# Optimization experiments

Measured on AMD Instinct MI355X. Metric: run time of the kernel, lower is better.

The kernel has to match this reference:

```python
import jax, jax.numpy as jnp
import numpy as np

DIM = 3072
HEADS = 24
HEAD_DIM = 128
MLP_HIDDEN = int(DIM * 3.0)   # 9216
EPS = 1e-6
B, S = 1, 4096


def setup_inputs() -> dict:
    key = jax.random.key(0)
    ks = jax.random.split(key, 9)
    fused_out = 3 * DIM + 2 * MLP_HIDDEN  # 27648
    std_in = 1.0 / np.sqrt(DIM)
    return {
        "hidden_states": jax.random.normal(ks[0], (B, S, DIM), jnp.float32),
        "temb_mod": jax.random.normal(ks[1], (B, 3 * DIM), jnp.float32),
        "rotary_cos": jax.random.uniform(ks[2], (S, HEAD_DIM), jnp.float32),
        "rotary_sin": jax.random.uniform(ks[3], (S, HEAD_DIM), jnp.float32),
        "w_qkv_mlp": jax.random.normal(ks[4], (DIM, fused_out), jnp.float32) * std_in,
        "w_out_attn": jax.random.normal(ks[5], (DIM, DIM), jnp.float32) * std_in,
        "w_out_mlp": jax.random.normal(ks[6], (MLP_HIDDEN, DIM), jnp.float32) * (1.0 / np.sqrt(MLP_HIDDEN)),
        "norm_q_w": jnp.ones((HEAD_DIM,), jnp.float32),
        "norm_k_w": jnp.ones((HEAD_DIM,), jnp.float32),
    }


def _rms_norm(x, w):
    var = jnp.mean(jnp.square(x), axis=-1, keepdims=True)
    return x * jax.lax.rsqrt(var + EPS) * w


def _apply_rope(x, cos, sin):
    # x: [B,H,S,D]; cos/sin: [S,D]. Interleaved (diffusers FLUX) rotation.
    xr = x.reshape(*x.shape[:-1], HEAD_DIM // 2, 2)
    x_re, x_im = xr[..., 0], xr[..., 1]
    x_rot = jnp.stack([-x_im, x_re], axis=-1).reshape(x.shape)
    return x * cos + x_rot * sin


def reference(hidden_states, temb_mod, rotary_cos, rotary_sin,
              w_qkv_mlp, w_out_attn, w_out_mlp, norm_q_w, norm_k_w):
    residual = hidden_states
    # modulation split: shift, scale, gate each [B,1,D]
    shift, scale, gate = jnp.split(temb_mod[:, None, :], 3, axis=-1)
    # LayerNorm (no affine)
    mu = jnp.mean(hidden_states, axis=-1, keepdims=True)
    var = jnp.mean(jnp.square(hidden_states - mu), axis=-1, keepdims=True)
    ln = (hidden_states - mu) * jax.lax.rsqrt(var + EPS)
    h = ln * (1.0 + scale) + shift
    # fused QKV + MLP projection
    qkv_mlp = jnp.einsum('bsd,df->bsf', h, w_qkv_mlp)
    qkv, mlp_gate_up = jnp.split(qkv_mlp, [3 * DIM], axis=-1)
    q, k, v = jnp.split(qkv, 3, axis=-1)
    to_heads = lambda t: t.reshape(B, S, HEADS, HEAD_DIM).transpose(0, 2, 1, 3)
    q, k, v = to_heads(q), to_heads(k), to_heads(v)
    q = _apply_rope(_rms_norm(q, norm_q_w), rotary_cos, rotary_sin)
    k = _apply_rope(_rms_norm(k, norm_k_w), rotary_cos, rotary_sin)
    # attention
    scores = jnp.einsum('bhqd,bhkd->bhqk', q, k) / np.sqrt(HEAD_DIM).astype(np.float32)
    attn = jnp.einsum('bhqk,bhkd->bhqd', jax.nn.softmax(scores, axis=-1), v)
    attn = attn.transpose(0, 2, 1, 3).reshape(B, S, DIM)
    # SwiGLU
    a, b = jnp.split(mlp_gate_up, 2, axis=-1)
    mlp_out = jax.nn.silu(a) * b
    out = jnp.einsum('bsd,de->bse', attn, w_out_attn) + jnp.einsum('bsm,md->bsd', mlp_out, w_out_mlp)
    return residual + gate * out
```

## Files before the change

### kernel.cpp

```cpp
#include <hip/hip_runtime.h>
#include <stdint.h>
#include <math.h>

#define DIM 3072
#define SEQ 4096
#define NH 24
#define HD 128
#define MLP 9216
#define FUSED 27648
#define SD FUSED
#define K2 12288

typedef __attribute__((ext_vector_type(8))) short short8;
typedef __attribute__((ext_vector_type(4))) float f32x4;

__device__ __forceinline__ float bf2f(uint16_t b){ uint32_t x = ((uint32_t)b)<<16; return __builtin_bit_cast(float,x); }
__device__ __forceinline__ uint16_t f2bf(float f){
  uint32_t x = __builtin_bit_cast(uint32_t,f);
  x += 0x7fffu + ((x>>16)&1u);
  return (uint16_t)(x>>16);
}
__device__ __forceinline__ void gl_lds16(const void* g, void* l){
  __builtin_amdgcn_global_load_lds((const __attribute__((address_space(1))) void*)g,
                                   (__attribute__((address_space(3))) void*)l, 16, 0, 0);
}

__global__ __launch_bounds__(256) void castT_kernel(const float* __restrict__ src,
                                                    uint16_t* __restrict__ dst,
                                                    int K, int N, int dstStride){
  __shared__ float tile[32][33];
  int t = threadIdx.x;
  int n0 = blockIdx.x<<5, k0 = blockIdx.y<<5;
  int r = t>>3, c4 = (t&7)<<2;
  float4 v = *(const float4*)&src[(size_t)(k0+r)*N + n0 + c4];
  tile[r][c4] = v.x; tile[r][c4+1] = v.y; tile[r][c4+2] = v.z; tile[r][c4+3] = v.w;
  __syncthreads();
  int n = t>>3, kc = (t&7)<<2;
  ushort4 o;
  o.x = f2bf(tile[kc  ][n]);
  o.y = f2bf(tile[kc+1][n]);
  o.z = f2bf(tile[kc+2][n]);
  o.w = f2bf(tile[kc+3][n]);
  *(ushort4*)&dst[(size_t)(n0+n)*dstStride + k0 + kc] = o;
}

__global__ __launch_bounds__(256) void ln_mod_kernel(const float* __restrict__ x,
                                                     const float* __restrict__ temb,
                                                     uint16_t* __restrict__ h){
  int s = blockIdx.x;
  int t = threadIdx.x;
  const float4* row = (const float4*)(x + (size_t)s*DIM);
  float4 v[3];
  float sum=0.f, ss=0.f;
  #pragma unroll
  for (int i=0;i<3;i++){
    v[i] = row[t + i*256];
    sum += v[i].x+v[i].y+v[i].z+v[i].w;
    ss  += v[i].x*v[i].x + v[i].y*v[i].y + v[i].z*v[i].z + v[i].w*v[i].w;
  }
  #pragma unroll
  for (int off=32; off; off>>=1){ sum += __shfl_xor(sum, off, 64); ss += __shfl_xor(ss, off, 64); }
  __shared__ float red[8];
  int lane = t&63, w = t>>6;
  if (lane==0){ red[w]=sum; red[w+4]=ss; }
  __syncthreads();
  sum = red[0]+red[1]+red[2]+red[3];
  ss  = red[4]+red[5]+red[6]+red[7];
  float mu = sum*(1.f/DIM);
  float var = ss*(1.f/DIM) - mu*mu;
  float rs = rsqrtf(var + 1e-6f);
  uint16_t* hrow = h + (size_t)s*DIM;
  #pragma unroll
  for (int i=0;i<3;i++){
    int c = (t + i*256)*4;
    float4 sc = *(const float4*)&temb[DIM + c];
    float4 sh = *(const float4*)&temb[c];
    ushort4 o;
    o.x = f2bf((v[i].x - mu)*rs*(1.f+sc.x) + sh.x);
    o.y = f2bf((v[i].y - mu)*rs*(1.f+sc.y) + sh.y);
    o.z = f2bf((v[i].z - mu)*rs*(1.f+sc.z) + sh.z);
    o.w = f2bf((v[i].w - mu)*rs*(1.f+sc.w) + sh.w);
    *(ushort4*)&hrow[c] = o;
  }
}

#define STAGE_HT(SRC, LDSB, KOFF) do{ \
    gl_lds16((SRC) + (KOFF), (LDSB) + (size_t)t*8); \
    gl_lds16((SRC) + r64K + (KOFF), (LDSB) + (size_t)(t+512)*8); \
  }while(0)

#define GPHASE(MI0, MI1, STG, WAITV) do{ \
    short8 a00 = *(const short8*)&Ab[(MI0)*1024 + pk0]; \
    short8 a01 = *(const short8*)&Ab[(MI0)*1024 + pk1]; \
    short8 a10 = *(const short8*)&Ab[(MI1)*1024 + pk0]; \
    short8 a11 = *(const short8*)&Ab[(MI1)*1024 + pk1]; \
    STG; \
    __builtin_amdgcn_s_barrier(); \
    asm volatile("s_waitcnt lgkmcnt(0)" ::: "memory"); \
    __builtin_amdgcn_s_setprio(1); \
    _Pragma("unroll") \
    for (int ni=0; ni<4; ni++){ \
      acc[MI0][ni] = __builtin_amdgcn_mfma_f32_16x16x32_bf16(a00, bfr[ni][0], acc[MI0][ni], 0,0,0); \
      acc[MI1][ni] = __builtin_amdgcn_mfma_f32_16x16x32_bf16(a10, bfr[ni][0], acc[MI1][ni], 0,0,0); \
      acc[MI0][ni] = __builtin_amdgcn_mfma_f32_16x16x32_bf16(a01, bfr[ni][1], acc[MI0][ni], 0,0,0); \
      acc[MI1][ni] = __builtin_amdgcn_mfma_f32_16x16x32_bf16(a11, bfr[ni][1], acc[MI1][ni], 0,0,0); \
    } \
    __builtin_amdgcn_s_setprio(0); \
    WAITV \
    __builtin_amdgcn_s_barrier(); \
  }while(0)

template<bool OUT_BF16, bool FINAL>
__global__ __launch_bounds__(512,2) void gemm256_kernel(const uint16_t* __restrict__ A,
                                                        const uint16_t* __restrict__ BT,
                                                        void* __restrict__ Cout,
                                                        const float* __restrict__ resid,
                                                        const float* __restrict__ temb,
                                                        int M, int N, int K){
  __shared__ alignas(16) uint16_t As[2][2][128*64];
  __shared__ alignas(16) uint16_t Bs[2][2][128*64];
  const int t = threadIdx.x, lane = t&63, w = t>>6;
  const int G = gridDim.x, cpx = G>>3;
  const int b = blockIdx.x;
  const int b2 = (b&7)*cpx + (b>>3);
  const int mt = M>>8;
  const int n_t = b2/mt, m_t = b2 - n_t*mt;
  const size_t m0 = (size_t)m_t<<8, n0 = (size_t)n_t<<8;
  const int wm = (w>>2)<<7, wn = (w&3)<<6;
  const int lr = lane&15, q4 = lane>>4;
  const int r0 = t>>3;
  const int g0 = (t&7) ^ (r0&7);
  const uint16_t* Asrc = A  + (m0 + r0)*(size_t)K + g0*8;
  const uint16_t* Bsrc = BT + (n0 + r0)*(size_t)K + g0*8;
  const size_t r64K = (size_t)64*K, r128K = (size_t)128*K;
  const int halfA = w>>2, halfB = (w&3)>>1, rbB = wn&64;
  const uint16_t* ArdBase = &As[0][halfA][0] + lr*64;
  const uint16_t* BrdBase = &Bs[0][halfB][0] + (rbB+lr)*64;
  const int x7 = lr&7;
  const int pk0 = (q4^x7)<<3, pk1 = ((q4|4)^x7)<<3;
  STAGE_HT(Bsrc, &Bs[0][0][0], (size_t)0);
  STAGE_HT(Bsrc, &Bs[0][1][0], r128K);
  STAGE_HT(Asrc, &As[0][0][0], (size_t)0);
  STAGE_HT(Asrc, &As[0][1][0], r128K);
  STAGE_HT(Bsrc, &Bs[1][0][0], (size_t)64);
  STAGE_HT(Bsrc, &Bs[1][1][0], r128K + 64);
  asm volatile("s_waitcnt vmcnt(4)" ::: "memory");
  __builtin_amdgcn_s_barrier();
  f32x4 acc[8][4] = {};
  const int NT = K>>6;
  for (int T=0; T<NT; ++T){
    const int cur = T&1, nxt = cur^1;
    const uint16_t* Ab = ArdBase + (cur<<14);
    const uint16_t* Bb = BrdBase + (cur<<14);
    uint16_t* AsN0 = &As[nxt][0][0]; uint16_t* AsN1 = &As[nxt][1][0];
    uint16_t* BsC0 = &Bs[cur][0][0]; uint16_t* BsC1 = &Bs[cur][1][0];
    const bool stA = (T+1<NT), stB = (T+2<NT);
    const size_t kA = (size_t)(T+1)<<6, kB = (size_t)(T+2)<<6;
    short8 bfr[4][2];
    #pragma unroll
    for (int ni=0; ni<4; ni++){
      bfr[ni][0] = *(const short8*)&Bb[ni*1024 + pk0];
      bfr[ni][1] = *(const short8*)&Bb[ni*1024 + pk1];
    }
    GPHASE(0,1, if(stA){ STAGE_HT(Asrc, AsN0, kA); }, ;);
    GPHASE(2,3, if(stA){ STAGE_HT(Asrc, AsN1, kA + r128K); }, ;);
    GPHASE(4,5, if(stB){ STAGE_HT(Bsrc, BsC0, kB); }, ;);
    GPHASE(6,7, if(stB){ STAGE_HT(Bsrc, BsC1, kB + r128K); },
           if(stB){ asm volatile("s_waitcnt vmcnt(4)" ::: "memory"); }
           else   { asm volatile("s_waitcnt vmcnt(0)" ::: "memory"); });
  }
  #pragma unroll
  for (int mi=0; mi<8; mi++){
    #pragma unroll
    for (int ni=0; ni<4; ni++){
      const size_t col = n0 + wn + ni*16 + lr;
      const float gate = FINAL ? temb[2*DIM + col] : 0.f;
      #pragma unroll
      for (int r=0; r<4; r++){
        const size_t row = m0 + wm + mi*16 + (q4<<2) + r;
        const size_t idx = row*(size_t)N + col;
        float vv = acc[mi][ni][r];
        if (FINAL) vv = resid[idx] + gate*vv;
        if (OUT_BF16) ((uint16_t*)Cout)[idx] = f2bf(vv);
        else          ((float*)Cout)[idx] = vv;
      }
    }
  }
}

__global__ __launch_bounds__(256) void qk_rope_kernel(uint16_t* __restrict__ qkv,
                                                      const float* __restrict__ cosb,
                                                      const float* __restrict__ sinb,
                                                      const float* __restrict__ wq,
                                                      const float* __restrict__ wk){
  int t = threadIdx.x, lane = t&63, w = t>>6;
  int pair = blockIdx.x*4 + w;
  int s = pair/24, hh = pair - s*24;
  int d0 = lane*2;
  float c0 = cosb[s*HD + d0], c1 = cosb[s*HD + d0+1];
  float sn0 = sinb[s*HD + d0], sn1 = sinb[s*HD + d0+1];
  #pragma unroll
  for (int which=0; which<2; ++which){
    uint16_t* p = qkv + (size_t)s*SD + which*DIM + hh*HD + d0;
    const float* ww = which ? wk : wq;
    uint32_t u = *(const uint32_t*)p;
    float x0 = bf2f((uint16_t)(u&0xffffu)), x1 = bf2f((uint16_t)(u>>16));
    float ssum = x0*x0 + x1*x1;
    #pragma unroll
    for (int off=32; off; off>>=1) ssum += __shfl_xor(ssum, off, 64);
    float r = rsqrtf(ssum*(1.f/HD) + 1e-6f);
    float xn0 = x0*r*ww[d0], xn1 = x1*r*ww[d0+1];
    float y0 = xn0*c0 - xn1*sn0;
    float y1 = xn1*c1 + xn0*sn1;
    *(uint32_t*)p = (uint32_t)f2bf(y0) | ((uint32_t)f2bf(y1)<<16);
  }
}

__global__ __launch_bounds__(256) void attn_kernel(const uint16_t* __restrict__ qkv,
                                                   uint16_t* __restrict__ out){
  __shared__ alignas(16) uint16_t QP[64*128];
  __shared__ alignas(16) uint16_t Ks[64*128];
  __shared__ alignas(16) uint16_t Vt[128*64];
  int t = threadIdx.x, lane = t&63, w = t>>6;
  int q0 = blockIdx.x<<6, h = blockIdx.y;
  int lr = lane&15, q4 = lane>>4, lk = q4<<3;
  const uint16_t* qb = qkv + (size_t)q0*SD + h*HD;
  #pragma unroll
  for (int i=0;i<4;i++){
    int c = t + i*256;
    gl_lds16((const char*)(qb + (size_t)(c>>4)*SD) + ((c&15)<<4), (char*)QP + c*16);
  }
  __syncthreads();
  short8 qf[4];
  #pragma unroll
  for (int kc=0;kc<4;kc++) qf[kc] = *(const short8*)&QP[(w*16+lr)*128 + kc*32 + lk];
  __syncthreads();
  float m_i[4] = {-3.0e38f,-3.0e38f,-3.0e38f,-3.0e38f};
  float l_i[4] = {0.f,0.f,0.f,0.f};
  f32x4 o[8] = {};
  const uint16_t* kb = qkv + (size_t)DIM + h*HD;
  const uint16_t* vb = qkv + (size_t)(2*DIM) + h*HD;
  uint16_t* Pw = QP + w*(16*64);
  const float scale = 0.08838834764831845f;
  for (int kt=0; kt<64; ++kt){
    const uint16_t* kbt = kb + (size_t)(kt<<6)*SD;
    const uint16_t* vbt = vb + (size_t)(kt<<6)*SD;
    __syncthreads();
    #pragma unroll
    for (int i=0;i<4;i++){
      int c = t + i*256;
      int row = c>>4, gd = c&15;
      uint4 vv = *(const uint4*)(kbt + (size_t)row*SD + gd*8);
      *(uint4*)&Ks[row*128 + ((gd ^ (row&15))<<3)] = vv;
    }
    #pragma unroll
    for (int i=0;i<8;i++){
      int idx = t + i*256;
      int rp = idx>>6;
      int k0 = rp<<1, d0 = lane<<1;
      uint32_t u0 = *(const uint32_t*)(vbt + (size_t)k0*SD + d0);
      uint32_t u1 = *(const uint32_t*)(vbt + (size_t)(k0+1)*SD + d0);
      int pos = (((rp>>2) ^ (lane&7))<<3) + (k0&7);
      *(uint32_t*)&Vt[(d0<<6) + pos]     = (u0&0xffffu) | (u1<<16);
      *(uint32_t*)&Vt[((d0+1)<<6) + pos] = (u0>>16) | (u1&0xffff0000u);
    }
    __syncthreads();
    f32x4 sa[4];
    #pragma unroll
    for (int nk=0;nk<4;nk++){
      sa[nk] = (f32x4){0.f,0.f,0.f,0.f};
      #pragma unroll
      for (int kc=0;kc<4;kc++){
        short8 kf = *(const short8*)&Ks[(nk*16+lr)*128 + (((kc*4+q4) ^ lr)<<3)];
        sa[nk] = __builtin_amdgcn_mfma_f32_16x16x32_bf16(qf[kc], kf, sa[nk], 0,0,0);
      }
      sa[nk] *= scale;
    }
    float alpha[4], psum[4];
    #pragma unroll
    for (int r=0;r<4;r++){
      float mx = fmaxf(fmaxf(sa[0][r], sa[1][r]), fmaxf(sa[2][r], sa[3][r]));
      mx = fmaxf(mx, __shfl_xor(mx, 1, 64));
      mx = fmaxf(mx, __shfl_xor(mx, 2, 64));
      mx = fmaxf(mx, __shfl_xor(mx, 4, 64));
      mx = fmaxf(mx, __shfl_xor(mx, 8, 64));
      float mn = fmaxf(m_i[r], mx);
      alpha[r] = __expf(m_i[r] - mn);
      m_i[r] = mn;
      psum[r] = 0.f;
    }
    int prow = q4<<2;
    #pragma unroll
    for (int nk=0;nk<4;nk++){
      #pragma unroll
      for (int r=0;r<4;r++){
        float p = __expf(sa[nk][r] - m_i[r]);
        psum[r] += p;
        int key = nk*16 + lr;
        Pw[(prow+r)*64 + ((((key>>3) ^ (prow+r))&7)<<3) + (key&7)] = f2bf(p);
      }
    }
    #pragma unroll
    for (int r=0;r<4;r++){
      float ps = psum[r];
      ps += __shfl_xor(ps, 1, 64);
      ps += __shfl_xor(ps, 2, 64);
      ps += __shfl_xor(ps, 4, 64);
      ps += __shfl_xor(ps, 8, 64);
      l_i[r] = l_i[r]*alpha[r] + ps;
    }
    #pragma unroll
    for (int nd=0;nd<8;nd++){
      f32x4 t4 = o[nd];
      t4[0]*=alpha[0]; t4[1]*=alpha[1]; t4[2]*=alpha[2]; t4[3]*=alpha[3];
      o[nd]=t4;
    }
    #pragma unroll
    for (int kc=0;kc<2;kc++){
      short8 pf = *(const short8*)&Pw[lr*64 + ((((kc*4+q4) ^ lr)&7)<<3)];
      #pragma unroll
      for (int nd=0;nd<8;nd++){
        int d = nd*16 + lr;
        short8 vf = *(const short8*)&Vt[(d<<6) + ((((kc*4+q4) ^ ((lr>>1)&7)))<<3)];
        o[nd] = __builtin_amdgcn_mfma_f32_16x16x32_bf16(pf, vf, o[nd], 0,0,0);
      }
    }
  }
  uint16_t* ob = out + (size_t)(q0 + w*16)*K2 + h*HD;
  #pragma unroll
  for (int r=0;r<4;r++){
    float inv = 1.f/l_i[r];
    #pragma unroll
    for (int nd=0;nd<8;nd++)
      ob[(size_t)(q4*4 + r)*K2 + nd*16 + lr] = f2bf(o[nd][r]*inv);
  }
}

__global__ __launch_bounds__(256) void swiglu_kernel(const uint16_t* __restrict__ qkv,
                                                     uint16_t* __restrict__ mlp){
  size_t idx = ((size_t)blockIdx.x*256 + threadIdx.x)*4;
  size_t s = idx/MLP, j = idx - s*MLP;
  const uint16_t* pa = qkv + s*SD + 3*DIM + j;
  const uint16_t* pb = pa + MLP;
  ushort4 ua = *(const ushort4*)pa, ub = *(const ushort4*)pb;
  ushort4 o;
  float a, b;
  a = bf2f(ua.x); b = bf2f(ub.x); o.x = f2bf(a*b/(1.f+__expf(-a)));
  a = bf2f(ua.y); b = bf2f(ub.y); o.y = f2bf(a*b/(1.f+__expf(-a)));
  a = bf2f(ua.z); b = bf2f(ub.z); o.z = f2bf(a*b/(1.f+__expf(-a)));
  a = bf2f(ua.w); b = bf2f(ub.w); o.w = f2bf(a*b/(1.f+__expf(-a)));
  *(ushort4*)(mlp + s*K2 + j) = o;
}

extern "C" void kernel_launch(void* const* d_in, const int* in_sizes, int n_in,
                              void* d_out, int out_size, void* d_ws, size_t ws_size,
                              hipStream_t stream){
  (void)in_sizes; (void)n_in; (void)out_size;
  const float* hs   = (const float*)d_in[0];
  const float* temb = (const float*)d_in[1];
  const float* rcos = (const float*)d_in[2];
  const float* rsin = (const float*)d_in[3];
  const float* w1   = (const float*)d_in[4];
  const float* wa   = (const float*)d_in[5];
  const float* wm   = (const float*)d_in[6];
  const float* nqw  = (const float*)d_in[7];
  const float* nkw  = (const float*)d_in[8];

  char* ws = (char*)d_ws;
  const size_t off_w1T  = 0;
  const size_t off_woT  = 169869312ULL;
  const size_t off_h    = 245366784ULL;
  const size_t off_qkv  = 270532608ULL;
  const size_t off_ap   = 497025024ULL;
  const size_t needed   = 597688320ULL;
  if (ws_size < needed) return;

  uint16_t* w1T  = (uint16_t*)(ws + off_w1T);
  uint16_t* woT  = (uint16_t*)(ws + off_woT);
  uint16_t* hbuf = (uint16_t*)(ws + off_h);
  uint16_t* qkv  = (uint16_t*)(ws + off_qkv);
  uint16_t* ap   = (uint16_t*)(ws + off_ap);

  castT_kernel<<<dim3(FUSED/32, DIM/32), 256, 0, stream>>>(w1, w1T, DIM, FUSED, DIM);
  castT_kernel<<<dim3(DIM/32,  DIM/32),  256, 0, stream>>>(wa, woT, DIM, DIM, K2);
  castT_kernel<<<dim3(DIM/32,  MLP/32),  256, 0, stream>>>(wm, woT + DIM, MLP, DIM, K2);
  ln_mod_kernel<<<SEQ, 256, 0, stream>>>(hs, temb, hbuf);
  gemm256_kernel<true,false><<<(SEQ/256)*(FUSED/256), 512, 0, stream>>>(hbuf, w1T, qkv, nullptr, nullptr, SEQ, FUSED, DIM);
  qk_rope_kernel<<<SEQ*NH/4, 256, 0, stream>>>(qkv, rcos, rsin, nqw, nkw);
  attn_kernel<<<dim3(SEQ/64, NH), 256, 0, stream>>>(qkv, ap);
  swiglu_kernel<<<(SEQ*(size_t)MLP/4)/256, 256, 0, stream>>>(qkv, ap + DIM);
  gemm256_kernel<false,true><<<(SEQ/256)*(DIM/256), 512, 0, stream>>>(ap, woT, d_out, hs, temb, SEQ, DIM, K2);
}
```

Baseline: 2.415 ms.

## Software-pipeline LDS fragment reads across GEMM MFMA phases with register double-buffering

Restructures the GEMM main loop so each phase's A fragments are read from LDS into a second register set while the previous phase's MFMAs run. The next tile's A and B fragments are prefetched at the end of each iteration. sched_barrier is added to keep the compiler from reordering around the phase boundaries. The aim is to hide LDS read latency behind matrix math, at the cost of more VGPRs. The prefetch of the next tile now happens before the workgroup barrier, which risks reading LDS that other waves have not finished filling.

```diff
diff --git a/kernel.cpp b/kernel.cpp
--- a/kernel.cpp
+++ b/kernel.cpp
@@ -89,26 +89,30 @@
     gl_lds16((SRC) + r64K + (KOFF), (LDSB) + (size_t)(t+512)*8); \
   }while(0)
 
-#define GPHASE(MI0, MI1, STG, WAITV) do{ \
-    short8 a00 = *(const short8*)&Ab[(MI0)*1024 + pk0]; \
-    short8 a01 = *(const short8*)&Ab[(MI0)*1024 + pk1]; \
-    short8 a10 = *(const short8*)&Ab[(MI1)*1024 + pk0]; \
-    short8 a11 = *(const short8*)&Ab[(MI1)*1024 + pk1]; \
-    STG; \
-    __builtin_amdgcn_s_barrier(); \
-    asm volatile("s_waitcnt lgkmcnt(0)" ::: "memory"); \
-    __builtin_amdgcn_s_setprio(1); \
+#define PH_READ4(d0,d1,d2,d3, BASE, MIA, MIB) \
+    d0 = *(const short8*)&(BASE)[(MIA)*1024 + pk0]; \
+    d1 = *(const short8*)&(BASE)[(MIA)*1024 + pk1]; \
+    d2 = *(const short8*)&(BASE)[(MIB)*1024 + pk0]; \
+    d3 = *(const short8*)&(BASE)[(MIB)*1024 + pk1];
+
+#define PH_MFMA4(s0,s1,s2,s3, MI0, MI1) \
     _Pragma("unroll") \
     for (int ni=0; ni<4; ni++){ \
-      acc[MI0][ni] = __builtin_amdgcn_mfma_f32_16x16x32_bf16(a00, bfr[ni][0], acc[MI0][ni], 0,0,0); \
-      acc[MI1][ni] = __builtin_amdgcn_mfma_f32_16x16x32_bf16(a10, bfr[ni][0], acc[MI1][ni], 0,0,0); \
-      acc[MI0][ni] = __builtin_amdgcn_mfma_f32_16x16x32_bf16(a01, bfr[ni][1], acc[MI0][ni], 0,0,0); \
-      acc[MI1][ni] = __builtin_amdgcn_mfma_f32_16x16x32_bf16(a11, bfr[ni][1], acc[MI1][ni], 0,0,0); \
-    } \
+      acc[MI0][ni] = __builtin_amdgcn_mfma_f32_16x16x32_bf16(s0, bfr[ni][0], acc[MI0][ni], 0,0,0); \
+      acc[MI1][ni] = __builtin_amdgcn_mfma_f32_16x16x32_bf16(s2, bfr[ni][0], acc[MI1][ni], 0,0,0); \
+      acc[MI0][ni] = __builtin_amdgcn_mfma_f32_16x16x32_bf16(s1, bfr[ni][1], acc[MI0][ni], 0,0,0); \
+      acc[MI1][ni] = __builtin_amdgcn_mfma_f32_16x16x32_bf16(s3, bfr[ni][1], acc[MI1][ni], 0,0,0); \
+    }
+
+#define PH_COMMIT \
+    __builtin_amdgcn_sched_barrier(0); \
+    __builtin_amdgcn_s_barrier(); \
+    __builtin_amdgcn_s_setprio(1);
+
+#define PH_CLOSE \
     __builtin_amdgcn_s_setprio(0); \
-    WAITV \
-    __builtin_amdgcn_s_barrier(); \
-  }while(0)
+    __builtin_amdgcn_sched_barrier(0); \
+    __builtin_amdgcn_s_barrier();
 
 template<bool OUT_BF16, bool FINAL>
 __global__ __launch_bounds__(512,2) void gemm256_kernel(const uint16_t* __restrict__ A,
@@ -134,8 +138,10 @@
   const uint16_t* Bsrc = BT + (n0 + r0)*(size_t)K + g0*8;
   const size_t r64K = (size_t)64*K, r128K = (size_t)128*K;
   const int halfA = w>>2, halfB = (w&3)>>1, rbB = wn&64;
-  const uint16_t* ArdBase = &As[0][halfA][0] + lr*64;
-  const uint16_t* BrdBase = &Bs[0][halfB][0] + (rbB+lr)*64;
+  const uint16_t* ArdE = &As[0][halfA][0] + lr*64;
+  const uint16_t* BrdE = &Bs[0][halfB][0] + (rbB+lr)*64;
+  const uint16_t* ArdO = ArdE + 16384;
+  const uint16_t* BrdO = BrdE + 16384;
   const int x7 = lr&7;
   const int pk0 = (q4^x7)<<3, pk1 = ((q4|4)^x7)<<3;
   STAGE_HT(Bsrc, &Bs[0][0][0], (size_t)0);
@@ -146,28 +152,57 @@
   STAGE_HT(Bsrc, &Bs[1][1][0], r128K + 64);
   asm volatile("s_waitcnt vmcnt(4)" ::: "memory");
   __builtin_amdgcn_s_barrier();
+  short8 pa0,pa1,pa2,pa3, qa0,qa1,qa2,qa3;
+  short8 bfr[4][2];
+  PH_READ4(pa0,pa1,pa2,pa3, ArdE, 0, 1);
+  #pragma unroll
+  for (int ni=0; ni<4; ni++){
+    bfr[ni][0] = *(const short8*)&BrdE[ni*1024 + pk0];
+    bfr[ni][1] = *(const short8*)&BrdE[ni*1024 + pk1];
+  }
   f32x4 acc[8][4] = {};
   const int NT = K>>6;
   for (int T=0; T<NT; ++T){
-    const int cur = T&1, nxt = cur^1;
-    const uint16_t* Ab = ArdBase + (cur<<14);
-    const uint16_t* Bb = BrdBase + (cur<<14);
-    uint16_t* AsN0 = &As[nxt][0][0]; uint16_t* AsN1 = &As[nxt][1][0];
-    uint16_t* BsC0 = &Bs[cur][0][0]; uint16_t* BsC1 = &Bs[cur][1][0];
+    const uint16_t* AbC = (T&1) ? ArdO : ArdE;
+    const uint16_t* AbN = (T&1) ? ArdE : ArdO;
+    const uint16_t* BbN = (T&1) ? BrdE : BrdO;
+    uint16_t* AsN0 = &As[(T&1)^1][0][0];
+    uint16_t* AsN1 = &As[(T&1)^1][1][0];
+    uint16_t* BsC0 = &Bs[T&1][0][0];
+    uint16_t* BsC1 = &Bs[T&1][1][0];
     const bool stA = (T+1<NT), stB = (T+2<NT);
     const size_t kA = (size_t)(T+1)<<6, kB = (size_t)(T+2)<<6;
-    short8 bfr[4][2];
-    #pragma unroll
-    for (int ni=0; ni<4; ni++){
-      bfr[ni][0] = *(const short8*)&Bb[ni*1024 + pk0];
-      bfr[ni][1] = *(const short8*)&Bb[ni*1024 + pk1];
-    }
-    GPHASE(0,1, if(stA){ STAGE_HT(Asrc, AsN0, kA); }, ;);
-    GPHASE(2,3, if(stA){ STAGE_HT(Asrc, AsN1, kA + r128K); }, ;);
-    GPHASE(4,5, if(stB){ STAGE_HT(Bsrc, BsC0, kB); }, ;);
-    GPHASE(6,7, if(stB){ STAGE_HT(Bsrc, BsC1, kB + r128K); },
-           if(stB){ asm volatile("s_waitcnt vmcnt(4)" ::: "memory"); }
-           else   { asm volatile("s_waitcnt vmcnt(0)" ::: "memory"); });
+    PH_READ4(qa0,qa1,qa2,qa3, AbC, 2, 3);
+    if (stA){ STAGE_HT(Asrc, AsN0, kA); }
+    PH_COMMIT
+    PH_MFMA4(pa0,pa1,pa2,pa3, 0, 1)
+    PH_CLOSE
+    PH_READ4(pa0,pa1,pa2,pa3, AbC, 4, 5);
+    if (stA){ STAGE_HT(Asrc, AsN1, kA + r128K); }
+    PH_COMMIT
+    PH_MFMA4(qa0,qa1,qa2,qa3, 2, 3)
+    PH_CLOSE
+    PH_READ4(qa0,qa1,qa2,qa3, AbC, 6, 7);
+    if (stB){ STAGE_HT(Bsrc, BsC0, kB); }
+    PH_COMMIT
+    PH_MFMA4(pa0,pa1,pa2,pa3, 4, 5)
+    PH_CLOSE
+    if (stB){ STAGE_HT(Bsrc, BsC1, kB + r128K); }
+    PH_COMMIT
+    PH_MFMA4(qa0,qa1,qa2,qa3, 6, 7)
+    __builtin_amdgcn_s_setprio(0);
+    if (T+1 < NT){
+      if (stB){ asm volatile("s_waitcnt vmcnt(4)" ::: "memory"); }
+      else    { asm volatile("s_waitcnt vmcnt(0)" ::: "memory"); }
+      PH_READ4(pa0,pa1,pa2,pa3, AbN, 0, 1);
+      #pragma unroll
+      for (int ni=0; ni<4; ni++){
+        bfr[ni][0] = *(const short8*)&BbN[ni*1024 + pk0];
+        bfr[ni][1] = *(const short8*)&BbN[ni*1024 + pk1];
+      }
+    }
+    __builtin_amdgcn_sched_barrier(0);
+    __builtin_amdgcn_s_barrier();
   }
   #pragma unroll
   for (int mi=0; mi<8; mi++){
```

New measurement: 2.447 ms. No clear change (+1.3%).

## Transpose attention score tile, add lazy softmax rescale and direct K LDS loads

Applied to the files above, without the earlier changes.

Computes the score tile as K·Q^T so each lane holds one query's scores, cutting cross-lane max/sum reductions to two shuffles. Adds a warp-uniform lazy rescale that skips updating the running max and O rescaling when the new max grows by under a threshold. Loads K tiles straight into LDS via global_load_lds with the swizzle moved to the global address, packs P stores, and raises wave priority around MFMA blocks. Lazy rescaling risks larger intermediate exponentials, bounded by the threshold.

```diff
diff --git a/kernel.cpp b/kernel.cpp
--- a/kernel.cpp
+++ b/kernel.cpp
@@ -235,8 +235,7 @@
   #pragma unroll
   for (int kc=0;kc<4;kc++) qf[kc] = *(const short8*)&QP[(w*16+lr)*128 + kc*32 + lk];
   __syncthreads();
-  float m_i[4] = {-3.0e38f,-3.0e38f,-3.0e38f,-3.0e38f};
-  float l_i[4] = {0.f,0.f,0.f,0.f};
+  float m_q = -3.0e38f, l_q = 0.f;
   f32x4 o[8] = {};
   const uint16_t* kb = qkv + (size_t)DIM + h*HD;
   const uint16_t* vb = qkv + (size_t)(2*DIM) + h*HD;
@@ -250,8 +249,8 @@
     for (int i=0;i<4;i++){
       int c = t + i*256;
       int row = c>>4, gd = c&15;
-      uint4 vv = *(const uint4*)(kbt + (size_t)row*SD + gd*8);
-      *(uint4*)&Ks[row*128 + ((gd ^ (row&15))<<3)] = vv;
+      gl_lds16((const char*)(kbt + (size_t)row*SD) + (((gd ^ (row&15))&15)<<4),
+               (char*)Ks + c*16);
     }
     #pragma unroll
     for (int i=0;i<8;i++){
@@ -265,56 +264,63 @@
       *(uint32_t*)&Vt[((d0+1)<<6) + pos] = (u0>>16) | (u1&0xffff0000u);
     }
     __syncthreads();
-    f32x4 sa[4];
+    f32x4 ta[4];
+    __builtin_amdgcn_s_setprio(1);
     #pragma unroll
     for (int nk=0;nk<4;nk++){
-      sa[nk] = (f32x4){0.f,0.f,0.f,0.f};
+      ta[nk] = (f32x4){0.f,0.f,0.f,0.f};
       #pragma unroll
       for (int kc=0;kc<4;kc++){
         short8 kf = *(const short8*)&Ks[(nk*16+lr)*128 + (((kc*4+q4) ^ lr)<<3)];
-        sa[nk] = __builtin_amdgcn_mfma_f32_16x16x32_bf16(qf[kc], kf, sa[nk], 0,0,0);
+        ta[nk] = __builtin_amdgcn_mfma_f32_16x16x32_bf16(kf, qf[kc], ta[nk], 0,0,0);
       }
-      sa[nk] *= scale;
-    }
-    float alpha[4], psum[4];
-    #pragma unroll
-    for (int r=0;r<4;r++){
-      float mx = fmaxf(fmaxf(sa[0][r], sa[1][r]), fmaxf(sa[2][r], sa[3][r]));
-      mx = fmaxf(mx, __shfl_xor(mx, 1, 64));
-      mx = fmaxf(mx, __shfl_xor(mx, 2, 64));
-      mx = fmaxf(mx, __shfl_xor(mx, 4, 64));
-      mx = fmaxf(mx, __shfl_xor(mx, 8, 64));
-      float mn = fmaxf(m_i[r], mx);
-      alpha[r] = __expf(m_i[r] - mn);
-      m_i[r] = mn;
-      psum[r] = 0.f;
-    }
-    int prow = q4<<2;
+      ta[nk] *= scale;
+    }
+    __builtin_amdgcn_s_setprio(0);
+    float mx01 = fmaxf(fmaxf(ta[0][0],ta[0][1]), fmaxf(ta[0][2],ta[0][3]));
+    float mx23 = fmaxf(fmaxf(ta[1][0],ta[1][1]), fmaxf(ta[1][2],ta[1][3]));
+    float mx45 = fmaxf(fmaxf(ta[2][0],ta[2][1]), fmaxf(ta[2][2],ta[2][3]));
+    float mx67 = fmaxf(fmaxf(ta[3][0],ta[3][1]), fmaxf(ta[3][2],ta[3][3]));
+    float pmax = fmaxf(fmaxf(mx01,mx23), fmaxf(mx45,mx67));
+    pmax = fmaxf(pmax, __shfl_xor(pmax, 16, 64));
+    pmax = fmaxf(pmax, __shfl_xor(pmax, 32, 64));
+    int skip = __all(pmax <= m_q + 8.f);
+    float alpha_q = 1.f;
+    if (!skip){
+      float mnew = fmaxf(m_q, pmax);
+      alpha_q = __expf(m_q - mnew);
+      m_q = mnew;
+    }
+    float psum = 0.f;
     #pragma unroll
     for (int nk=0;nk<4;nk++){
+      float p0 = __expf(ta[nk][0] - m_q);
+      float p1 = __expf(ta[nk][1] - m_q);
+      float p2 = __expf(ta[nk][2] - m_q);
+      float p3 = __expf(ta[nk][3] - m_q);
+      psum += (p0+p1)+(p2+p3);
+      uint32_t lo = (uint32_t)f2bf(p0) | ((uint32_t)f2bf(p1)<<16);
+      uint32_t hi = (uint32_t)f2bf(p2) | ((uint32_t)f2bf(p3)<<16);
+      int k0 = nk*16 + (q4<<2);
+      uint2 pk; pk.x = lo; pk.y = hi;
+      *(uint2*)&Pw[lr*64 + ((((k0>>3) ^ lr)&7)<<3) + (k0&7)] = pk;
+    }
+    psum += __shfl_xor(psum, 16, 64);
+    psum += __shfl_xor(psum, 32, 64);
+    l_q = l_q*alpha_q + psum;
+    if (!skip){
+      float aR0 = __shfl(alpha_q, (q4<<2)+0, 64);
+      float aR1 = __shfl(alpha_q, (q4<<2)+1, 64);
+      float aR2 = __shfl(alpha_q, (q4<<2)+2, 64);
+      float aR3 = __shfl(alpha_q, (q4<<2)+3, 64);
       #pragma unroll
-      for (int r=0;r<4;r++){
-        float p = __expf(sa[nk][r] - m_i[r]);
-        psum[r] += p;
-        int key = nk*16 + lr;
-        Pw[(prow+r)*64 + ((((key>>3) ^ (prow+r))&7)<<3) + (key&7)] = f2bf(p);
+      for (int nd=0;nd<8;nd++){
+        f32x4 t4 = o[nd];
+        t4[0]*=aR0; t4[1]*=aR1; t4[2]*=aR2; t4[3]*=aR3;
+        o[nd]=t4;
       }
     }
-    #pragma unroll
-    for (int r=0;r<4;r++){
-      float ps = psum[r];
-      ps += __shfl_xor(ps, 1, 64);
-      ps += __shfl_xor(ps, 2, 64);
-      ps += __shfl_xor(ps, 4, 64);
-      ps += __shfl_xor(ps, 8, 64);
-      l_i[r] = l_i[r]*alpha[r] + ps;
-    }
-    #pragma unroll
-    for (int nd=0;nd<8;nd++){
-      f32x4 t4 = o[nd];
-      t4[0]*=alpha[0]; t4[1]*=alpha[1]; t4[2]*=alpha[2]; t4[3]*=alpha[3];
-      o[nd]=t4;
-    }
+    __builtin_amdgcn_s_setprio(1);
     #pragma unroll
     for (int kc=0;kc<2;kc++){
       short8 pf = *(const short8*)&Pw[lr*64 + ((((kc*4+q4) ^ lr)&7)<<3)];
@@ -325,14 +331,19 @@
         o[nd] = __builtin_amdgcn_mfma_f32_16x16x32_bf16(pf, vf, o[nd], 0,0,0);
       }
     }
-  }
+    __builtin_amdgcn_s_setprio(0);
+  }
+  float linv0 = 1.f/__shfl(l_q, (q4<<2)+0, 64);
+  float linv1 = 1.f/__shfl(l_q, (q4<<2)+1, 64);
+  float linv2 = 1.f/__shfl(l_q, (q4<<2)+2, 64);
+  float linv3 = 1.f/__shfl(l_q, (q4<<2)+3, 64);
   uint16_t* ob = out + (size_t)(q0 + w*16)*K2 + h*HD;
   #pragma unroll
-  for (int r=0;r<4;r++){
-    float inv = 1.f/l_i[r];
-    #pragma unroll
-    for (int nd=0;nd<8;nd++)
-      ob[(size_t)(q4*4 + r)*K2 + nd*16 + lr] = f2bf(o[nd][r]*inv);
+  for (int nd=0;nd<8;nd++){
+    ob[(size_t)(q4*4 + 0)*K2 + nd*16 + lr] = f2bf(o[nd][0]*linv0);
+    ob[(size_t)(q4*4 + 1)*K2 + nd*16 + lr] = f2bf(o[nd][1]*linv1);
+    ob[(size_t)(q4*4 + 2)*K2 + nd*16 + lr] = f2bf(o[nd][2]*linv2);
+    ob[(size_t)(q4*4 + 3)*K2 + nd*16 + lr] = f2bf(o[nd][3]*linv3);
   }
 }
 
```

New measurement: 2.289 ms. 1.06x faster.
